# Kernel tuning notes

Hardware: AMD Instinct MI355X
Metric: run time of the kernel (lower is better)

## Reference

```python
import jax, jax.numpy as jnp
import numpy as np

N_NODES = 100000
N_EDGES = 1600000
N_FEAT = 128
HIDDEN = 128
N_GRAPHS = 256
N_CLASSES = 2
BN_EPS = 1e-5


def _graph_conv(x, src, dst, W_rel, b_rel, W_root):
    # PyG GraphConv (aggr='add'): out_i = W_rel @ sum_{j->i} x_j + b_rel + W_root @ x_i
    agg = jax.ops.segment_sum(x[src], dst, num_segments=x.shape[0])  # [N, C_in]
    return agg @ W_rel + x @ W_root + b_rel


def _batch_norm(x, gamma, beta):
    # training-mode BN over node axis
    mean = jnp.mean(x, axis=0)
    var = jnp.var(x, axis=0)
    return (x - mean) * jax.lax.rsqrt(var + BN_EPS) * gamma + beta


def setup_inputs() -> dict:
    key = jax.random.key(0)
    ks = jax.random.split(key, 16)
    x = jax.random.normal(ks[0], (N_NODES, N_FEAT), dtype=jnp.float32)
    edge_index = jax.random.randint(ks[1], (2, N_EDGES), 0, N_NODES, dtype=jnp.int32)
    batch = jnp.sort(jax.random.randint(ks[2], (N_NODES,), 0, N_GRAPHS, dtype=jnp.int32))

    def glorot(k, fan_in, fan_out):
        s = jnp.sqrt(2.0 / (fan_in + fan_out)).astype(jnp.float32)
        return jax.random.normal(k, (fan_in, fan_out), dtype=jnp.float32) * s

    inp = {"x": x, "edge_index": edge_index, "batch": batch}
    dims = [(N_FEAT, HIDDEN), (HIDDEN, HIDDEN), (HIDDEN, HIDDEN)]
    for i, (fi, fo) in enumerate(dims, start=1):
        inp[f"W{i}r"] = glorot(ks[2 * i + 1], fi, fo)
        inp[f"b{i}"] = jnp.zeros((fo,), dtype=jnp.float32)
        inp[f"W{i}root"] = glorot(ks[2 * i + 2], fi, fo)
        inp[f"g{i}"] = jnp.ones((fo,), dtype=jnp.float32)
        inp[f"be{i}"] = jnp.zeros((fo,), dtype=jnp.float32)
    inp["Wlin"] = glorot(ks[10], HIDDEN, N_CLASSES)
    inp["blin"] = jnp.zeros((N_CLASSES,), dtype=jnp.float32)
    return inp


def reference(x, edge_index, batch,
              W1r, b1, W1root, g1, be1,
              W2r, b2, W2root, g2, be2,
              W3r, b3, W3root, g3, be3,
              Wlin, blin):
    src, dst = edge_index[0], edge_index[1]
    # dropout layers are identity in eval; BN uses batch statistics
    h = _graph_conv(x, src, dst, W1r, b1, W1root)
    h = _batch_norm(jax.nn.relu(h), g1, be1)
    h = _graph_conv(h, src, dst, W2r, b2, W2root)
    h = _batch_norm(jax.nn.relu(h), g2, be2)
    h = _graph_conv(h, src, dst, W3r, b3, W3root)
    h = _batch_norm(h, g3, be3)  # note: no relu on third conv, matching source
    # global_mean_pool over graphs
    sums = jax.ops.segment_sum(h, batch, num_segments=N_GRAPHS)          # [G, H]
    counts = jax.ops.segment_sum(jnp.ones((h.shape[0], 1), h.dtype), batch,
                                 num_segments=N_GRAPHS)                  # [G, 1]
    pooled = sums / jnp.maximum(counts, 1.0)
    return pooled @ Wlin + blin  # [G, n_classes]
```

## Files before the change

### kernel.cpp

```cpp
#include <hip/hip_runtime.h>
#include <math.h>
#include <stdint.h>

#define TPB 256
#define NF 128
#define BN_EPS_C 1e-5f
#define BSH 9
#define PE_EPB 4096

typedef __attribute__((ext_vector_type(8))) short bf16x8;
typedef __attribute__((ext_vector_type(4))) float f32x4;

__device__ __forceinline__ void atomAddF(float* p, float v) {
    unsafeAtomicAdd(p, v);
}

__device__ __forceinline__ short f2bf(float f) {
    unsigned u = __float_as_uint(f);
    unsigned r = (u + 0x7FFFu + ((u >> 16) & 1u)) >> 16;
    return (short)r;
}
__device__ __forceinline__ float bf2f(short b) {
    return __uint_as_float(((unsigned)(unsigned short)b) << 16);
}
__device__ __forceinline__ float bflo(unsigned u) { return __uint_as_float(u << 16); }
__device__ __forceinline__ float bfhi(unsigned u) { return __uint_as_float(u & 0xffff0000u); }
__device__ __forceinline__ unsigned packbf(float lo, float hi) {
    return (unsigned)(unsigned short)f2bf(lo) | ((unsigned)(unsigned short)f2bf(hi) << 16);
}

__device__ __forceinline__ void async_copy16u(const unsigned short* g, unsigned short* l) {
    __builtin_amdgcn_global_load_lds(
        (const __attribute__((address_space(1))) unsigned int*)g,
        (__attribute__((address_space(3))) unsigned int*)l, 16, 0, 0);
}

__global__ __launch_bounds__(TPB) void bucket_count(
    const int* __restrict__ dst, int* __restrict__ bucket_cnt, int E, int nbuck)
{
    __shared__ int h[256];
    h[threadIdx.x] = 0;
    __syncthreads();
    int base = blockIdx.x * PE_EPB;
    int lim = min(base + PE_EPB, E);
    for (int i = base + threadIdx.x; i < lim; i += 256)
        atomicAdd(&h[dst[i] >> BSH], 1);
    __syncthreads();
    if (threadIdx.x < nbuck && h[threadIdx.x])
        atomicAdd(&bucket_cnt[threadIdx.x], h[threadIdx.x]);
}

__global__ __launch_bounds__(TPB) void bucket_scan(
    const int* __restrict__ bucket_cnt, int* __restrict__ boff,
    int* __restrict__ bucket_cur, int nbuck, int E)
{
    __shared__ int s[256];
    int t = threadIdx.x;
    int v = (t < nbuck) ? bucket_cnt[t] : 0;
    s[t] = v;
    __syncthreads();
    for (int off = 1; off < 256; off <<= 1) {
        int x = (t >= off) ? s[t - off] : 0;
        __syncthreads();
        s[t] += x;
        __syncthreads();
    }
    int excl = s[t] - v;
    if (t < nbuck) { boff[t] = excl; bucket_cur[t] = excl; }
    if (t == 0) boff[nbuck] = E;
}

__global__ __launch_bounds__(TPB) void partition_edges(
    const int* __restrict__ src, const int* __restrict__ dst,
    int* __restrict__ bucket_cur, int2* __restrict__ pairs, int E, int nbuck)
{
    __shared__ int cnt[256];
    __shared__ int gbase[256];
    int t = threadIdx.x;
    cnt[t] = 0;
    __syncthreads();
    int base = blockIdx.x * PE_EPB;
    int myb[16], myrank[16], mys[16], myd[16];
#pragma unroll
    for (int j = 0; j < 16; ++j) {
        int i = base + j * 256 + t;
        if (i < E) {
            int d = dst[i];
            int b = d >> BSH;
            myb[j] = b; myd[j] = d; mys[j] = src[i];
            myrank[j] = atomicAdd(&cnt[b], 1);
        } else myb[j] = -1;
    }
    __syncthreads();
    if (t < nbuck && cnt[t]) gbase[t] = atomicAdd(&bucket_cur[t], cnt[t]);
    __syncthreads();
#pragma unroll
    for (int j = 0; j < 16; ++j)
        if (myb[j] >= 0)
            pairs[gbase[myb[j]] + myrank[j]] = make_int2(mys[j], myd[j]);
}

__global__ __launch_bounds__(TPB) void bucket_build(
    const int2* __restrict__ pairs, const int* __restrict__ boff,
    int* __restrict__ rowptr, int* __restrict__ srcs,
    float* __restrict__ degf, int M, int E)
{
    __shared__ int ldeg[512];
    __shared__ int lsum[256];
    int b = blockIdx.x;
    int t = threadIdx.x;
    int n0 = b << BSH;
    int nn = min(512, M - n0);
    int p0 = boff[b], p1 = boff[b + 1];
    ldeg[t] = 0; ldeg[t + 256] = 0;
    __syncthreads();
    for (int i = p0 + t; i < p1; i += 256)
        atomicAdd(&ldeg[pairs[i].y - n0], 1);
    __syncthreads();
    int a0 = ldeg[2 * t], a1 = ldeg[2 * t + 1];
    lsum[t] = a0 + a1;
    __syncthreads();
    for (int off = 1; off < 256; off <<= 1) {
        int x = (t >= off) ? lsum[t - off] : 0;
        __syncthreads();
        lsum[t] += x;
        __syncthreads();
    }
    int excl = lsum[t] - (a0 + a1);
    ldeg[2 * t]     = p0 + excl;
    ldeg[2 * t + 1] = p0 + excl + a0;
    if (2 * t < nn)     { rowptr[n0 + 2 * t]     = p0 + excl;      degf[n0 + 2 * t]     = (float)a0; }
    if (2 * t + 1 < nn) { rowptr[n0 + 2 * t + 1] = p0 + excl + a0; degf[n0 + 2 * t + 1] = (float)a1; }
    if (b == 0 && t == 0) rowptr[M] = E;
    __syncthreads();
    for (int i = p0 + t; i < p1; i += 256) {
        int2 pr = pairs[i];
        int pos = atomicAdd(&ldeg[pr.y - n0], 1);
        srcs[pos] = pr.x;
    }
}

__global__ __launch_bounds__(TPB) void cvt_bf16(
    const float* __restrict__ x, unsigned short* __restrict__ xb, int n8)
{
    int i = blockIdx.x * TPB + threadIdx.x;
    if (i >= n8) return;
    const f32x4* p = (const f32x4*)(x + (size_t)i * 8);
    f32x4 v0 = p[0], v1 = p[1];
    uint4 o;
    o.x = packbf(v0.x, v0.y); o.y = packbf(v0.z, v0.w);
    o.z = packbf(v1.x, v1.y); o.w = packbf(v1.z, v1.w);
    *(uint4*)(xb + (size_t)i * 8) = o;
}

__device__ __forceinline__ void acc8(float* a, uint4 r) {
    a[0] += bflo(r.x); a[1] += bfhi(r.x);
    a[2] += bflo(r.y); a[3] += bfhi(r.y);
    a[4] += bflo(r.z); a[5] += bfhi(r.z);
    a[6] += bflo(r.w); a[7] += bfhi(r.w);
}
__device__ __forceinline__ void acc8m(float* a, uint4 r, float m) {
    a[0] = fmaf(m, bflo(r.x), a[0]); a[1] = fmaf(m, bfhi(r.x), a[1]);
    a[2] = fmaf(m, bflo(r.y), a[2]); a[3] = fmaf(m, bfhi(r.y), a[3]);
    a[4] = fmaf(m, bflo(r.z), a[4]); a[5] = fmaf(m, bfhi(r.z), a[5]);
    a[6] = fmaf(m, bflo(r.w), a[6]); a[7] = fmaf(m, bfhi(r.w), a[7]);
}

__global__ __launch_bounds__(TPB) void gather_bf16(
    const unsigned short* __restrict__ hb, const int* __restrict__ rowptr,
    const int* __restrict__ srcs,
    unsigned short* __restrict__ agg_hi, unsigned short* __restrict__ agg_lo, int M)
{
    int wid = (blockIdx.x * TPB + threadIdx.x) >> 6;
    if (wid >= M) return;
    int lane = threadIdx.x & 63;
    int grp  = lane >> 4;
    int li   = lane & 15;
    int start = rowptr[wid], end = rowptr[wid + 1];

    float a0[8] = {0, 0, 0, 0, 0, 0, 0, 0};
    float a1[8] = {0, 0, 0, 0, 0, 0, 0, 0};
    int e = start;
    for (; e + 7 < end; e += 8) {
        int s0 = srcs[e + grp];
        int s1 = srcs[e + 4 + grp];
        uint4 r0 = *(const uint4*)(hb + (size_t)s0 * NF + li * 8);
        uint4 r1 = *(const uint4*)(hb + (size_t)s1 * NF + li * 8);
        acc8(a0, r0);
        acc8(a1, r1);
    }
    for (; e < end; e += 4) {
        int idx = e + grp;
        int s = srcs[min(idx, end - 1)];
        uint4 r = *(const uint4*)(hb + (size_t)s * NF + li * 8);
        float m = (idx < end) ? 1.0f : 0.0f;
        acc8m(a0, r, m);
    }
#pragma unroll
    for (int j = 0; j < 8; ++j) a0[j] += a1[j];
#pragma unroll
    for (int j = 0; j < 8; ++j) a0[j] += __shfl_xor(a0[j], 16);
#pragma unroll
    for (int j = 0; j < 8; ++j) a0[j] += __shfl_xor(a0[j], 32);
    if (lane < 16) {
        float h[8], l[8];
#pragma unroll
        for (int j = 0; j < 8; ++j) {
            h[j] = bf2f(f2bf(a0[j]));
            l[j] = a0[j] - h[j];
        }
        uint4 oh, ol;
        oh.x = packbf(h[0], h[1]); oh.y = packbf(h[2], h[3]);
        oh.z = packbf(h[4], h[5]); oh.w = packbf(h[6], h[7]);
        ol.x = packbf(l[0], l[1]); ol.y = packbf(l[2], l[3]);
        ol.z = packbf(l[4], l[5]); ol.w = packbf(l[6], l[7]);
        *(uint4*)(agg_hi + (size_t)wid * NF + li * 8) = oh;
        *(uint4*)(agg_lo + (size_t)wid * NF + li * 8) = ol;
    }
}

__device__ __forceinline__ void wpack_store(
    unsigned short* __restrict__ wpk, int n, int k, float w)
{
    short h = f2bf(w);
    short l = f2bf(w - bf2f(h));
    int kc = k >> 5, grp = (k >> 3) & 3, el = k & 7;
    int base = kc * 8192 + n * 64;
    wpk[base + ((grp      ) ^ (n & 7)) * 8 + el] = (unsigned short)h;
    wpk[base + ((grp ^ 4) ^ (n & 7)) * 8 + el] = (unsigned short)l;
}

__global__ __launch_bounds__(256) void wsplit_kernel(
    const float* __restrict__ Wr, const float* __restrict__ Wo,
    unsigned short* __restrict__ wpk)
{
    int n = blockIdx.x;
    int k = threadIdx.x;
    float v = (k < NF) ? Wr[k * NF + n] : Wo[(k - NF) * NF + n];
    wpack_store(wpk, n, k, v);
}

__global__ __launch_bounds__(256) void fold_kernel(
    const float* __restrict__ a, const float* __restrict__ c,
    const float* __restrict__ Wr, const float* __restrict__ Wo,
    const float* __restrict__ b,
    unsigned short* __restrict__ wpk,
    float* __restrict__ bias2, float* __restrict__ dvec)
{
    __shared__ float red[256];
    int n = blockIdx.x;
    int k = threadIdx.x;
    float w, contrib;
    if (k < NF) { w = Wr[k * NF + n];          contrib = c[k] * w;       w *= a[k]; }
    else        { int kk = k - NF; w = Wo[kk * NF + n]; contrib = c[kk] * w; w *= a[kk]; }
    wpack_store(wpk, n, k, w);
    red[k] = contrib;
    __syncthreads();
    for (int off = 64; off >= 1; off >>= 1) {
        if ((k & 127) < off) red[k] += red[k + off];
        __syncthreads();
    }
    if (k == 0)   dvec[n]  = red[0];
    if (k == 128) bias2[n] = b[n] + red[128];
}

template<bool RELU, bool NORM>
__global__ __launch_bounds__(TPB) void gemm_mfma(
    const unsigned short* __restrict__ Ahi, const unsigned short* __restrict__ Alo,
    const unsigned short* Ax,
    const unsigned short* __restrict__ wpk,
    const float* __restrict__ bias, const float* __restrict__ dvec,
    const float* __restrict__ degf, unsigned short* C,
    float* __restrict__ gsum, float* __restrict__ gsq, int M)
{
    __shared__ unsigned short sW[8192];

    const int tid  = threadIdx.x;
    const int wid  = tid >> 6;
    const int lane = tid & 63;
    const int lg   = lane >> 4;
    const int ln   = lane & 15;
    const int rowbase = blockIdx.x * 128 + wid * 32;

    f32x4 acc[2][8];
#pragma unroll
    for (int i = 0; i < 2; ++i)
#pragma unroll
        for (int j = 0; j < 8; ++j) acc[i][j] = (f32x4){0.f, 0.f, 0.f, 0.f};

    size_t aoff[2];
#pragma unroll
    for (int mt = 0; mt < 2; ++mt)
        aoff[mt] = (size_t)min(rowbase + mt * 16 + ln, M - 1) * NF + lg * 8;

    {
#pragma unroll
        for (int it = 0; it < 4; ++it) {
            int seg = it * 256 + tid;
            async_copy16u(wpk + seg * 8, sW + seg * 8);
        }
    }
    bf16x8 aH[2], aL[2], nH[2], nL[2];
#pragma unroll
    for (int mt = 0; mt < 2; ++mt) {
        aH[mt] = *(const bf16x8*)(Ahi + aoff[mt]);
        aL[mt] = *(const bf16x8*)(Alo + aoff[mt]);
    }

#pragma unroll
    for (int kc = 0; kc < 8; ++kc) {
        __syncthreads();

        if (kc < 3) {
#pragma unroll
            for (int mt = 0; mt < 2; ++mt) {
                nH[mt] = *(const bf16x8*)(Ahi + aoff[mt] + (kc + 1) * 32);
                nL[mt] = *(const bf16x8*)(Alo + aoff[mt] + (kc + 1) * 32);
            }
        } else if (kc < 7) {
#pragma unroll
            for (int mt = 0; mt < 2; ++mt)
                nH[mt] = *(const bf16x8*)(Ax + aoff[mt] + (kc - 3) * 32);
        }

#pragma unroll
        for (int nt = 0; nt < 8; ++nt) {
            int n = nt * 16 + ln;
            int boff = n * 64 + ((lg ^ (n & 7)) << 3);
            bf16x8 bhi = *(const bf16x8*)(sW + boff);
            bf16x8 blo = *(const bf16x8*)(sW + (boff ^ 32));
            if (kc < 4) {
#pragma unroll
                for (int mt = 0; mt < 2; ++mt) {
                    acc[mt][nt] = __builtin_amdgcn_mfma_f32_16x16x32_bf16(aH[mt], bhi, acc[mt][nt], 0, 0, 0);
                    acc[mt][nt] = __builtin_amdgcn_mfma_f32_16x16x32_bf16(aL[mt], bhi, acc[mt][nt], 0, 0, 0);
                    acc[mt][nt] = __builtin_amdgcn_mfma_f32_16x16x32_bf16(aH[mt], blo, acc[mt][nt], 0, 0, 0);
                }
            } else {
#pragma unroll
                for (int mt = 0; mt < 2; ++mt) {
                    acc[mt][nt] = __builtin_amdgcn_mfma_f32_16x16x32_bf16(aH[mt], bhi, acc[mt][nt], 0, 0, 0);
                    acc[mt][nt] = __builtin_amdgcn_mfma_f32_16x16x32_bf16(aH[mt], blo, acc[mt][nt], 0, 0, 0);
                }
            }
        }

        __syncthreads();
        if (kc < 7) {
            const unsigned short* src = wpk + (kc + 1) * 8192;
#pragma unroll
            for (int it = 0; it < 4; ++it) {
                int seg = it * 256 + tid;
                async_copy16u(src + seg * 8, sW + seg * 8);
            }
        }
#pragma unroll
        for (int mt = 0; mt < 2; ++mt) { aH[mt] = nH[mt]; aL[mt] = nL[mt]; }
    }

    float B_[8], D_[8];
#pragma unroll
    for (int nt = 0; nt < 8; ++nt) {
        B_[nt] = bias[nt * 16 + ln];
        D_[nt] = NORM ? dvec[nt * 16 + ln] : 0.f;
    }
    float s8[8], q8[8];
#pragma unroll
    for (int nt = 0; nt < 8; ++nt) { s8[nt] = 0.f; q8[nt] = 0.f; }

#pragma unroll
    for (int mt = 0; mt < 2; ++mt) {
#pragma unroll
        for (int r = 0; r < 4; ++r) {
            int row = rowbase + mt * 16 + lg * 4 + r;
            if (row < M) {
                float dg = NORM ? degf[row] : 0.f;
#pragma unroll
                for (int nt = 0; nt < 8; ++nt) {
                    float v = acc[mt][nt][r] + B_[nt];
                    if (NORM) v += dg * D_[nt];
                    if (RELU) v = fmaxf(v, 0.f);
                    C[(size_t)row * NF + nt * 16 + ln] = (unsigned short)f2bf(v);
                    s8[nt] += v;
                    q8[nt] += v * v;
                }
            }
        }
    }

    __syncthreads();
    float* ssum = (float*)sW;
    float* ssq  = ssum + 2048;
    const int rg = wid * 4 + lg;
#pragma unroll
    for (int nt = 0; nt < 8; ++nt) {
        ssum[rg * NF + nt * 16 + ln] = s8[nt];
        ssq [rg * NF + nt * 16 + ln] = q8[nt];
    }
    __syncthreads();
    if (tid < NF) {
        float s = 0.f, q = 0.f;
#pragma unroll
        for (int g = 0; g < 16; ++g) { s += ssum[g * NF + tid]; q += ssq[g * NF + tid]; }
        atomAddF(&gsum[tid], s);
        atomAddF(&gsq[tid], q);
    }
}

__global__ __launch_bounds__(128) void bn_finalize(
    const float* __restrict__ gsum, const float* __restrict__ gsq,
    const float* __restrict__ gamma, const float* __restrict__ beta,
    float* __restrict__ a, float* __restrict__ c, int M)
{
    int k = threadIdx.x;
    float invM = 1.0f / (float)M;
    float mean = gsum[k] * invM;
    float var  = fmaxf(gsq[k] * invM - mean * mean, 0.f);
    float s    = gamma[k] / sqrtf(var + BN_EPS_C);
    a[k] = s;
    c[k] = beta[k] - mean * s;
}

__global__ __launch_bounds__(TPB) void pool_kernel(
    const unsigned short* __restrict__ h, const int* __restrict__ batch,
    float* __restrict__ pooled, float* __restrict__ counts, int M)
{
    int base = blockIdx.x * 128;
    int col  = threadIdx.x & 127;
    int half = threadIdx.x >> 7;
    int end  = min(base + 128, M);
    float acc = 0.f; int cnt = 0; int gcur = -1;
    for (int n = base + half; n < end; n += 2) {
        int g = batch[n];
        if (g != gcur) {
            if (gcur >= 0) {
                atomAddF(&pooled[(size_t)gcur * NF + col], acc);
                if (col == 0) atomAddF(&counts[gcur], (float)cnt);
            }
            acc = 0.f; cnt = 0; gcur = g;
        }
        acc += bf2f((short)h[(size_t)n * NF + col]);
        cnt += 1;
    }
    if (gcur >= 0) {
        atomAddF(&pooled[(size_t)gcur * NF + col], acc);
        if (col == 0) atomAddF(&counts[gcur], (float)cnt);
    }
}

__global__ __launch_bounds__(TPB) void final_kernel(
    const float* __restrict__ pooled, const float* __restrict__ counts,
    const float* __restrict__ a3, const float* __restrict__ c3,
    const float* __restrict__ Wlin, const float* __restrict__ blin,
    float* __restrict__ out, int G)
{
    int g = threadIdx.x;
    if (g >= G) return;
    float cntRaw = counts[g];
    float inv = 1.0f / fmaxf(cntRaw, 1.0f);
    float nonEmpty = cntRaw > 0.5f ? 1.0f : 0.0f;
    float acc0 = 0.f, acc1 = 0.f;
    for (int k = 0; k < NF; ++k) {
        float v = (a3[k] * pooled[(size_t)g * NF + k] * inv + c3[k]) * nonEmpty;
        acc0 += v * Wlin[k * 2 + 0];
        acc1 += v * Wlin[k * 2 + 1];
    }
    out[g * 2 + 0] = acc0 + blin[0];
    out[g * 2 + 1] = acc1 + blin[1];
}

extern "C" void kernel_launch(void* const* d_in, const int* in_sizes, int n_in,
                              void* d_out, int out_size, void* d_ws, size_t ws_size,
                              hipStream_t stream)
{
    const float* x     = (const float*)d_in[0];
    const int*   eidx  = (const int*)d_in[1];
    const int*   batch = (const int*)d_in[2];
    const float* W1r = (const float*)d_in[3],  *b1 = (const float*)d_in[4];
    const float* W1o = (const float*)d_in[5],  *g1 = (const float*)d_in[6],  *be1 = (const float*)d_in[7];
    const float* W2r = (const float*)d_in[8],  *b2 = (const float*)d_in[9];
    const float* W2o = (const float*)d_in[10], *g2 = (const float*)d_in[11], *be2 = (const float*)d_in[12];
    const float* W3r = (const float*)d_in[13], *b3 = (const float*)d_in[14];
    const float* W3o = (const float*)d_in[15], *g3 = (const float*)d_in[16], *be3 = (const float*)d_in[17];
    const float* Wlin = (const float*)d_in[18], *blin = (const float*)d_in[19];
    float* out = (float*)d_out;

    const int M = in_sizes[0] / NF;
    const int E = in_sizes[1] / 2;
    const int G = out_size / 2;
    const int* src = eidx;
    const int* dst = eidx + E;
    const int nbuck = (M + 511) >> BSH;

    const size_t NODEF = (size_t)M * NF;

    unsigned short* agg_hi = (unsigned short*)d_ws;
    unsigned short* agg_lo = agg_hi + NODEF;
    unsigned short* xb     = agg_lo + NODEF;
    unsigned short* hb     = xb + NODEF;
    float* zf   = (float*)(hb + NODEF);
    float* gsum1 = zf;        float* gsq1 = zf + 128;
    float* gsum2 = zf + 256;  float* gsq2 = zf + 384;
    float* gsum3 = zf + 512;  float* gsq3 = zf + 640;
    float* counts = zf + 768;
    float* pooled = counts + G;
    int*   zi   = (int*)(pooled + (size_t)G * NF);
    int* bucket_cnt = zi;
    int* bucket_cur = zi + 256;
    int* boff       = zi + 512;
    int* ziEnd      = zi + 1024;
    float* ac = (float*)ziEnd;
    float* a1 = ac;       float* c1 = ac + 128;
    float* a2 = ac + 256; float* c2 = ac + 384;
    float* a3 = ac + 512; float* c3 = ac + 640;
    float* bias2_2 = ac + 768;  float* dvec2 = ac + 896;
    float* bias2_3 = ac + 1024; float* dvec3 = ac + 1152;
    int* rowptr = (int*)(ac + 1280);
    int* srcs   = rowptr + (M + 1);
    float* degf = (float*)(srcs + E);
    uintptr_t pp = ((uintptr_t)(degf + M) + 15) & ~(uintptr_t)15;
    int2* pairs = (int2*)pp;
    unsigned short* wpk1 = (unsigned short*)pp;
    unsigned short* wpk2 = wpk1 + 65536;
    unsigned short* wpk3 = wpk2 + 65536;

    const int gridEP       = (E + PE_EPB - 1) / PE_EPB;
    const int gatherBlocks = (int)(((size_t)M * 64 + TPB - 1) / TPB);
    const int gemmBlocks   = (M + 127) / 128;
    const int poolBlocks   = (M + 127) / 128;
    const int cvtBlocks    = (int)((NODEF / 8 + TPB - 1) / TPB);

    size_t zbytes = (char*)ziEnd - (char*)zf;
    hipMemsetAsync(zf, 0, zbytes, stream);

    bucket_count   <<<gridEP, TPB, 0, stream>>>(dst, bucket_cnt, E, nbuck);
    bucket_scan    <<<1, TPB, 0, stream>>>(bucket_cnt, boff, bucket_cur, nbuck, E);
    partition_edges<<<gridEP, TPB, 0, stream>>>(src, dst, bucket_cur, pairs, E, nbuck);
    bucket_build   <<<nbuck, TPB, 0, stream>>>(pairs, boff, rowptr, srcs, degf, M, E);

    cvt_bf16<<<cvtBlocks, TPB, 0, stream>>>(x, xb, (int)(NODEF / 8));

    wsplit_kernel<<<128, 256, 0, stream>>>(W1r, W1o, wpk1);
    gather_bf16<<<gatherBlocks, TPB, 0, stream>>>(xb, rowptr, srcs, agg_hi, agg_lo, M);
    gemm_mfma<true, false><<<gemmBlocks, TPB, 0, stream>>>(
        agg_hi, agg_lo, xb, wpk1, b1, nullptr, nullptr, hb, gsum1, gsq1, M);
    bn_finalize<<<1, 128, 0, stream>>>(gsum1, gsq1, g1, be1, a1, c1, M);

    fold_kernel<<<128, 256, 0, stream>>>(a1, c1, W2r, W2o, b2, wpk2, bias2_2, dvec2);
    gather_bf16<<<gatherBlocks, TPB, 0, stream>>>(hb, rowptr, srcs, agg_hi, agg_lo, M);
    gemm_mfma<true, true><<<gemmBlocks, TPB, 0, stream>>>(
        agg_hi, agg_lo, hb, wpk2, bias2_2, dvec2, degf, hb, gsum2, gsq2, M);
    bn_finalize<<<1, 128, 0, stream>>>(gsum2, gsq2, g2, be2, a2, c2, M);

    fold_kernel<<<128, 256, 0, stream>>>(a2, c2, W3r, W3o, b3, wpk3, bias2_3, dvec3);
    gather_bf16<<<gatherBlocks, TPB, 0, stream>>>(hb, rowptr, srcs, agg_hi, agg_lo, M);
    gemm_mfma<false, true><<<gemmBlocks, TPB, 0, stream>>>(
        agg_hi, agg_lo, hb, wpk3, bias2_3, dvec3, degf, hb, gsum3, gsq3, M);
    bn_finalize<<<1, 128, 0, stream>>>(gsum3, gsq3, g3, be3, a3, c3, M);

    pool_kernel<<<poolBlocks, TPB, 0, stream>>>(hb, batch, pooled, counts, M);
    final_kernel<<<1, TPB, 0, stream>>>(pooled, counts, a3, c3, Wlin, blin, out, G);
}
```

Baseline: 554.3 us.

## Fuse BN finalize into consumers, pack edge pairs, widen gather unroll

Removes the three bn_finalize launches by computing BN scale/shift inline in fold_kernel and final_kernel. Edge partitioning now packs src and the local dst offset into one 32-bit int instead of an int2, halving the intermediate traffic; this assumes node ids fit in 17 bits. The gather loop is unrolled to 16 edges per iteration with four packed float2 accumulators, and the masked tail is replaced by a predicated load. The aim is fewer kernel launches and more memory-level parallelism in the gather, at the cost of more registers.

```diff
diff --git a/kernel.cpp b/kernel.cpp
--- a/kernel.cpp
+++ b/kernel.cpp
@@ -10,6 +10,7 @@
 
 typedef __attribute__((ext_vector_type(8))) short bf16x8;
 typedef __attribute__((ext_vector_type(4))) float f32x4;
+typedef __attribute__((ext_vector_type(2))) float f32x2;
 
 __device__ __forceinline__ void atomAddF(float* p, float v) {
     unsafeAtomicAdd(p, v);
@@ -35,6 +36,15 @@
         (__attribute__((address_space(3))) unsigned int*)l, 16, 0, 0);
 }
 
+__device__ __forceinline__ void bn_ac(float gs, float gq, float gamma, float beta,
+                                      float invM, float* a, float* c) {
+    float mean = gs * invM;
+    float var  = fmaxf(gq * invM - mean * mean, 0.f);
+    float s    = gamma / sqrtf(var + BN_EPS_C);
+    *a = s;
+    *c = beta - mean * s;
+}
+
 __global__ __launch_bounds__(TPB) void bucket_count(
     const int* __restrict__ dst, int* __restrict__ bucket_cnt, int E, int nbuck)
 {
@@ -72,7 +82,7 @@
 
 __global__ __launch_bounds__(TPB) void partition_edges(
     const int* __restrict__ src, const int* __restrict__ dst,
-    int* __restrict__ bucket_cur, int2* __restrict__ pairs, int E, int nbuck)
+    int* __restrict__ bucket_cur, int* __restrict__ ppk, int E, int nbuck)
 {
     __shared__ int cnt[256];
     __shared__ int gbase[256];
@@ -80,14 +90,15 @@
     cnt[t] = 0;
     __syncthreads();
     int base = blockIdx.x * PE_EPB;
-    int myb[16], myrank[16], mys[16], myd[16];
+    int myb[16], myrank[16], myp[16];
 #pragma unroll
     for (int j = 0; j < 16; ++j) {
         int i = base + j * 256 + t;
         if (i < E) {
             int d = dst[i];
             int b = d >> BSH;
-            myb[j] = b; myd[j] = d; mys[j] = src[i];
+            myb[j] = b;
+            myp[j] = src[i] | ((d & 511) << 17);
             myrank[j] = atomicAdd(&cnt[b], 1);
         } else myb[j] = -1;
     }
@@ -97,11 +108,11 @@
 #pragma unroll
     for (int j = 0; j < 16; ++j)
         if (myb[j] >= 0)
-            pairs[gbase[myb[j]] + myrank[j]] = make_int2(mys[j], myd[j]);
+            ppk[gbase[myb[j]] + myrank[j]] = myp[j];
 }
 
 __global__ __launch_bounds__(TPB) void bucket_build(
-    const int2* __restrict__ pairs, const int* __restrict__ boff,
+    const int* __restrict__ ppk, const int* __restrict__ boff,
     int* __restrict__ rowptr, int* __restrict__ srcs,
     float* __restrict__ degf, int M, int E)
 {
@@ -115,7 +126,7 @@
     ldeg[t] = 0; ldeg[t + 256] = 0;
     __syncthreads();
     for (int i = p0 + t; i < p1; i += 256)
-        atomicAdd(&ldeg[pairs[i].y - n0], 1);
+        atomicAdd(&ldeg[ppk[i] >> 17], 1);
     __syncthreads();
     int a0 = ldeg[2 * t], a1 = ldeg[2 * t + 1];
     lsum[t] = a0 + a1;
@@ -134,9 +145,9 @@
     if (b == 0 && t == 0) rowptr[M] = E;
     __syncthreads();
     for (int i = p0 + t; i < p1; i += 256) {
-        int2 pr = pairs[i];
-        int pos = atomicAdd(&ldeg[pr.y - n0], 1);
-        srcs[pos] = pr.x;
+        int v = ppk[i];
+        int pos = atomicAdd(&ldeg[v >> 17], 1);
+        srcs[pos] = v & 0x1FFFF;
     }
 }
 
@@ -153,17 +164,11 @@
     *(uint4*)(xb + (size_t)i * 8) = o;
 }
 
-__device__ __forceinline__ void acc8(float* a, uint4 r) {
-    a[0] += bflo(r.x); a[1] += bfhi(r.x);
-    a[2] += bflo(r.y); a[3] += bfhi(r.y);
-    a[4] += bflo(r.z); a[5] += bfhi(r.z);
-    a[6] += bflo(r.w); a[7] += bfhi(r.w);
-}
-__device__ __forceinline__ void acc8m(float* a, uint4 r, float m) {
-    a[0] = fmaf(m, bflo(r.x), a[0]); a[1] = fmaf(m, bfhi(r.x), a[1]);
-    a[2] = fmaf(m, bflo(r.y), a[2]); a[3] = fmaf(m, bfhi(r.y), a[3]);
-    a[4] = fmaf(m, bflo(r.z), a[4]); a[5] = fmaf(m, bfhi(r.z), a[5]);
-    a[6] = fmaf(m, bflo(r.w), a[6]); a[7] = fmaf(m, bfhi(r.w), a[7]);
+__device__ __forceinline__ void accp(f32x2* a, uint4 r) {
+    a[0] += (f32x2){bflo(r.x), bfhi(r.x)};
+    a[1] += (f32x2){bflo(r.y), bfhi(r.y)};
+    a[2] += (f32x2){bflo(r.z), bfhi(r.z)};
+    a[3] += (f32x2){bflo(r.w), bfhi(r.w)};
 }
 
 __global__ __launch_bounds__(TPB) void gather_bf16(
@@ -177,37 +182,53 @@
     int grp  = lane >> 4;
     int li   = lane & 15;
     int start = rowptr[wid], end = rowptr[wid + 1];
-
-    float a0[8] = {0, 0, 0, 0, 0, 0, 0, 0};
-    float a1[8] = {0, 0, 0, 0, 0, 0, 0, 0};
+    const unsigned short* base = hb + li * 8;
+
+    f32x2 A0[4], A1[4], A2[4], A3[4];
+#pragma unroll
+    for (int j = 0; j < 4; ++j) {
+        A0[j] = (f32x2){0.f, 0.f}; A1[j] = A0[j]; A2[j] = A0[j]; A3[j] = A0[j];
+    }
+
     int e = start;
-    for (; e + 7 < end; e += 8) {
+    for (; e + 15 < end; e += 16) {
         int s0 = srcs[e + grp];
         int s1 = srcs[e + 4 + grp];
-        uint4 r0 = *(const uint4*)(hb + (size_t)s0 * NF + li * 8);
-        uint4 r1 = *(const uint4*)(hb + (size_t)s1 * NF + li * 8);
-        acc8(a0, r0);
-        acc8(a1, r1);
-    }
-    for (; e < end; e += 4) {
-        int idx = e + grp;
-        int s = srcs[min(idx, end - 1)];
-        uint4 r = *(const uint4*)(hb + (size_t)s * NF + li * 8);
-        float m = (idx < end) ? 1.0f : 0.0f;
-        acc8m(a0, r, m);
-    }
-#pragma unroll
-    for (int j = 0; j < 8; ++j) a0[j] += a1[j];
-#pragma unroll
-    for (int j = 0; j < 8; ++j) a0[j] += __shfl_xor(a0[j], 16);
-#pragma unroll
-    for (int j = 0; j < 8; ++j) a0[j] += __shfl_xor(a0[j], 32);
+        int s2 = srcs[e + 8 + grp];
+        int s3 = srcs[e + 12 + grp];
+        uint4 r0 = *(const uint4*)(base + (size_t)s0 * NF);
+        uint4 r1 = *(const uint4*)(base + (size_t)s1 * NF);
+        uint4 r2 = *(const uint4*)(base + (size_t)s2 * NF);
+        uint4 r3 = *(const uint4*)(base + (size_t)s3 * NF);
+        accp(A0, r0); accp(A1, r1); accp(A2, r2); accp(A3, r3);
+    }
+    for (; e + 3 < end; e += 4) {
+        int s = srcs[e + grp];
+        uint4 r = *(const uint4*)(base + (size_t)s * NF);
+        accp(A0, r);
+    }
+    int rem = end - e;
+    if (grp < rem) {
+        int s = srcs[e + grp];
+        uint4 r = *(const uint4*)(base + (size_t)s * NF);
+        accp(A1, r);
+    }
+
+#pragma unroll
+    for (int j = 0; j < 4; ++j) A0[j] = (A0[j] + A1[j]) + (A2[j] + A3[j]);
+    float v[8] = {A0[0].x, A0[0].y, A0[1].x, A0[1].y,
+                  A0[2].x, A0[2].y, A0[3].x, A0[3].y};
+#pragma unroll
+    for (int j = 0; j < 8; ++j) v[j] += __shfl_xor(v[j], 16);
+#pragma unroll
+    for (int j = 0; j < 8; ++j) v[j] += __shfl_xor(v[j], 32);
+
     if (lane < 16) {
         float h[8], l[8];
 #pragma unroll
         for (int j = 0; j < 8; ++j) {
-            h[j] = bf2f(f2bf(a0[j]));
-            l[j] = a0[j] - h[j];
+            h[j] = bf2f(f2bf(v[j]));
+            l[j] = v[j] - h[j];
         }
         uint4 oh, ol;
         oh.x = packbf(h[0], h[1]); oh.y = packbf(h[2], h[3]);
@@ -241,18 +262,22 @@
 }
 
 __global__ __launch_bounds__(256) void fold_kernel(
-    const float* __restrict__ a, const float* __restrict__ c,
+    const float* __restrict__ gsum, const float* __restrict__ gsq,
+    const float* __restrict__ gamma, const float* __restrict__ beta,
     const float* __restrict__ Wr, const float* __restrict__ Wo,
     const float* __restrict__ b,
     unsigned short* __restrict__ wpk,
-    float* __restrict__ bias2, float* __restrict__ dvec)
+    float* __restrict__ bias2, float* __restrict__ dvec, int M)
 {
     __shared__ float red[256];
     int n = blockIdx.x;
     int k = threadIdx.x;
-    float w, contrib;
-    if (k < NF) { w = Wr[k * NF + n];          contrib = c[k] * w;       w *= a[k]; }
-    else        { int kk = k - NF; w = Wo[kk * NF + n]; contrib = c[kk] * w; w *= a[kk]; }
+    int kk = k & 127;
+    float a, c;
+    bn_ac(gsum[kk], gsq[kk], gamma[kk], beta[kk], 1.0f / (float)M, &a, &c);
+    float w = (k < NF) ? Wr[k * NF + n] : Wo[kk * NF + n];
+    float contrib = c * w;
+    w *= a;
     wpack_store(wpk, n, k, w);
     red[k] = contrib;
     __syncthreads();
@@ -405,20 +430,6 @@
         atomAddF(&gsum[tid], s);
         atomAddF(&gsq[tid], q);
     }
-}
-
-__global__ __launch_bounds__(128) void bn_finalize(
-    const float* __restrict__ gsum, const float* __restrict__ gsq,
-    const float* __restrict__ gamma, const float* __restrict__ beta,
-    float* __restrict__ a, float* __restrict__ c, int M)
-{
-    int k = threadIdx.x;
-    float invM = 1.0f / (float)M;
-    float mean = gsum[k] * invM;
-    float var  = fmaxf(gsq[k] * invM - mean * mean, 0.f);
-    float s    = gamma[k] / sqrtf(var + BN_EPS_C);
-    a[k] = s;
-    c[k] = beta[k] - mean * s;
 }
 
 __global__ __launch_bounds__(TPB) void pool_kernel(
@@ -450,18 +461,27 @@
 
 __global__ __launch_bounds__(TPB) void final_kernel(
     const float* __restrict__ pooled, const float* __restrict__ counts,
-    const float* __restrict__ a3, const float* __restrict__ c3,
+    const float* __restrict__ gsum3, const float* __restrict__ gsq3,
+    const float* __restrict__ g3, const float* __restrict__ be3,
     const float* __restrict__ Wlin, const float* __restrict__ blin,
-    float* __restrict__ out, int G)
-{
-    int g = threadIdx.x;
+    float* __restrict__ out, int G, int M)
+{
+    __shared__ float sa[128], sc[128];
+    int t = threadIdx.x;
+    if (t < 128) {
+        float a, c;
+        bn_ac(gsum3[t], gsq3[t], g3[t], be3[t], 1.0f / (float)M, &a, &c);
+        sa[t] = a; sc[t] = c;
+    }
+    __syncthreads();
+    int g = t;
     if (g >= G) return;
     float cntRaw = counts[g];
     float inv = 1.0f / fmaxf(cntRaw, 1.0f);
     float nonEmpty = cntRaw > 0.5f ? 1.0f : 0.0f;
     float acc0 = 0.f, acc1 = 0.f;
     for (int k = 0; k < NF; ++k) {
-        float v = (a3[k] * pooled[(size_t)g * NF + k] * inv + c3[k]) * nonEmpty;
+        float v = (sa[k] * pooled[(size_t)g * NF + k] * inv + sc[k]) * nonEmpty;
         acc0 += v * Wlin[k * 2 + 0];
         acc1 += v * Wlin[k * 2 + 1];
     }
@@ -510,16 +530,13 @@
     int* boff       = zi + 512;
     int* ziEnd      = zi + 1024;
     float* ac = (float*)ziEnd;
-    float* a1 = ac;       float* c1 = ac + 128;
-    float* a2 = ac + 256; float* c2 = ac + 384;
-    float* a3 = ac + 512; float* c3 = ac + 640;
-    float* bias2_2 = ac + 768;  float* dvec2 = ac + 896;
-    float* bias2_3 = ac + 1024; float* dvec3 = ac + 1152;
-    int* rowptr = (int*)(ac + 1280);
+    float* bias2_2 = ac;        float* dvec2 = ac + 128;
+    float* bias2_3 = ac + 256;  float* dvec3 = ac + 384;
+    int* rowptr = (int*)(ac + 512);
     int* srcs   = rowptr + (M + 1);
     float* degf = (float*)(srcs + E);
     uintptr_t pp = ((uintptr_t)(degf + M) + 15) & ~(uintptr_t)15;
-    int2* pairs = (int2*)pp;
+    int* ppk = (int*)pp;
     unsigned short* wpk1 = (unsigned short*)pp;
     unsigned short* wpk2 = wpk1 + 65536;
     unsigned short* wpk3 = wpk2 + 65536;
@@ -535,8 +552,8 @@
 
     bucket_count   <<<gridEP, TPB, 0, stream>>>(dst, bucket_cnt, E, nbuck);
     bucket_scan    <<<1, TPB, 0, stream>>>(bucket_cnt, boff, bucket_cur, nbuck, E);
-    partition_edges<<<gridEP, TPB, 0, stream>>>(src, dst, bucket_cur, pairs, E, nbuck);
-    bucket_build   <<<nbuck, TPB, 0, stream>>>(pairs, boff, rowptr, srcs, degf, M, E);
+    partition_edges<<<gridEP, TPB, 0, stream>>>(src, dst, bucket_cur, ppk, E, nbuck);
+    bucket_build   <<<nbuck, TPB, 0, stream>>>(ppk, boff, rowptr, srcs, degf, M, E);
 
     cvt_bf16<<<cvtBlocks, TPB, 0, stream>>>(x, xb, (int)(NODEF / 8));
 
@@ -544,20 +561,20 @@
     gather_bf16<<<gatherBlocks, TPB, 0, stream>>>(xb, rowptr, srcs, agg_hi, agg_lo, M);
     gemm_mfma<true, false><<<gemmBlocks, TPB, 0, stream>>>(
         agg_hi, agg_lo, xb, wpk1, b1, nullptr, nullptr, hb, gsum1, gsq1, M);
-    bn_finalize<<<1, 128, 0, stream>>>(gsum1, gsq1, g1, be1, a1, c1, M);
-
-    fold_kernel<<<128, 256, 0, stream>>>(a1, c1, W2r, W2o, b2, wpk2, bias2_2, dvec2);
+
+    fold_kernel<<<128, 256, 0, stream>>>(gsum1, gsq1, g1, be1, W2r, W2o, b2,
+                                         wpk2, bias2_2, dvec2, M);
     gather_bf16<<<gatherBlocks, TPB, 0, stream>>>(hb, rowptr, srcs, agg_hi, agg_lo, M);
     gemm_mfma<true, true><<<gemmBlocks, TPB, 0, stream>>>(
         agg_hi, agg_lo, hb, wpk2, bias2_2, dvec2, degf, hb, gsum2, gsq2, M);
-    bn_finalize<<<1, 128, 0, stream>>>(gsum2, gsq2, g2, be2, a2, c2, M);
-
-    fold_kernel<<<128, 256, 0, stream>>>(a2, c2, W3r, W3o, b3, wpk3, bias2_3, dvec3);
+
+    fold_kernel<<<128, 256, 0, stream>>>(gsum2, gsq2, g2, be2, W3r, W3o, b3,
+                                         wpk3, bias2_3, dvec3, M);
     gather_bf16<<<gatherBlocks, TPB, 0, stream>>>(hb, rowptr, srcs, agg_hi, agg_lo, M);
     gemm_mfma<false, true><<<gemmBlocks, TPB, 0, stream>>>(
         agg_hi, agg_lo, hb, wpk3, bias2_3, dvec3, degf, hb, gsum3, gsq3, M);
-    bn_finalize<<<1, 128, 0, stream>>>(gsum3, gsq3, g3, be3, a3, c3, M);
 
     pool_kernel<<<poolBlocks, TPB, 0, stream>>>(hb, batch, pooled, counts, M);
-    final_kernel<<<1, TPB, 0, stream>>>(pooled, counts, a3, c3, Wlin, blin, out, G);
-}
+    final_kernel<<<1, TPB, 0, stream>>>(pooled, counts, gsum3, gsq3, g3, be3,
+                                        Wlin, blin, out, G, M);
+}
```

Result: slower. 572.1 us (+3.2%).
